# Optimization experiments

Measured on AMD Instinct MI355X. Metric: run time of the kernel, lower is better.

The kernel has to match this reference:

```python
import jax, jax.numpy as jnp
import numpy as np

N_NODES = 50000
N_EDGES = 800000
IN_DIM = 128
HIDDEN = 128
N_GRAPHS = 512


def setup_inputs() -> dict:
    key = jax.random.key(0)
    ks = jax.random.split(key, 9)
    x = jax.random.normal(ks[0], (N_NODES, IN_DIM), dtype=jnp.float32)
    edge_index = jax.random.randint(ks[1], (2, N_EDGES), 0, N_NODES, dtype=jnp.int32)
    batch = jnp.sort(jax.random.randint(ks[2], (N_NODES,), 0, N_GRAPHS, dtype=jnp.int32))
    # GCNConv params: linear (no bias) applied before propagation, bias added after.
    s1 = 1.0 / np.sqrt(IN_DIM)
    s2 = 1.0 / np.sqrt(HIDDEN)
    W1 = jax.random.uniform(ks[3], (IN_DIM, HIDDEN), jnp.float32, -s1, s1)
    b1 = jnp.zeros((HIDDEN,), jnp.float32)
    W2 = jax.random.uniform(ks[4], (HIDDEN, HIDDEN), jnp.float32, -s2, s2)
    b2 = jnp.zeros((HIDDEN,), jnp.float32)
    Wl = jax.random.uniform(ks[5], (HIDDEN, 1), jnp.float32, -s2, s2)
    bl = jax.random.uniform(ks[6], (1,), jnp.float32, -s2, s2)
    return {"x": x, "edge_index": edge_index, "batch": batch,
            "W1": W1, "b1": b1, "W2": W2, "b2": b2, "Wl": Wl, "bl": bl}


def gcn_conv(x, W, b, src, dst):
    # PyG GCNConv: h = D^{-1/2} (A + I) D^{-1/2} (x W) + b, with self-loops.
    h = x @ W                                        # [N, H]
    deg = jnp.zeros((N_NODES,), h.dtype).at[dst].add(1.0) + 1.0  # +1 for self-loop
    dinv = jax.lax.rsqrt(deg)                        # [N]
    msg = h[src] * (dinv[src] * dinv[dst])[:, None]  # [E, H] gather + normalize
    agg = jax.ops.segment_sum(msg, dst, num_segments=N_NODES)    # scatter-add
    agg = agg + h * (dinv * dinv)[:, None]           # self-loop contribution
    return agg + b


def reference(x, edge_index, batch, W1, b1, W2, b2, Wl, bl):
    src, dst = edge_index[0], edge_index[1]
    h = jax.nn.relu(gcn_conv(x, W1, b1, src, dst))
    h = jax.nn.relu(gcn_conv(h, W2, b2, src, dst))
    # global mean pool over graphs
    sums = jax.ops.segment_sum(h, batch, num_segments=N_GRAPHS)  # [G, H]
    cnt = jax.ops.segment_sum(jnp.ones((N_NODES,), h.dtype), batch, num_segments=N_GRAPHS)
    pooled = sums / jnp.maximum(cnt, 1.0)[:, None]
    return pooled @ Wl + bl
```

## Files before the change

kernel.cpp:

```cpp
#include <hip/hip_runtime.h>
#include <hip/hip_bf16.h>

#define N_NODES 50000
#define N_EDGES 800000
#define DIM 128
#define N_GRAPHS 512
#define NBUCK ((N_NODES + 63) / 64)
#define SC_CH 16384

typedef unsigned int uint;
typedef unsigned short ushort;
typedef __attribute__((ext_vector_type(8))) short short8;
typedef __attribute__((ext_vector_type(4))) float f32x4;

__device__ __forceinline__ ushort f2bf(float f) {
    uint u = __float_as_uint(f);
    uint r = (u + 0x7FFF + ((u >> 16) & 1)) >> 16;
    return (ushort)r;
}
__device__ __forceinline__ uint pack2(float a, float b) {
    return (uint)f2bf(a) | ((uint)f2bf(b) << 16);
}
__device__ __forceinline__ float2 unpack2(uint v) {
    return make_float2(__uint_as_float(v << 16), __uint_as_float(v & 0xFFFF0000u));
}


__global__ __launch_bounds__(256) void k_init(const float* __restrict__ W1,
                                              const float* __restrict__ W2,
                                              uint* __restrict__ wf1,
                                              uint* __restrict__ wf2,
                                              int* __restrict__ bucketCnt) {
    int t = blockIdx.x * 256 + threadIdx.x;
    if (t < NBUCK) bucketCnt[t] = 0;
    const float* W = (t < 8192) ? W1 : W2;
    uint* dst = (t < 8192) ? wf1 : wf2;
    int r = t & 8191;
    int j2 = r & 3;
    int lane = (r >> 2) & 63;
    int tk = r >> 8;
    int kc = tk & 3, ct = tk >> 2;
    int j = j2 * 2;
    int k = kc * 32 + (lane >> 4) * 8 + j;
    int n = ct * 16 + (lane & 15);
    dst[r] = pack2(W[k * 128 + n], W[(k + 1) * 128 + n]);
}


__global__ __launch_bounds__(1024) void k_bcount(const int* __restrict__ ei,
                                                 int* __restrict__ bucketCnt, int E) {
    __shared__ int h[NBUCK];
    int tid = threadIdx.x;
    for (int t = tid; t < NBUCK; t += 1024) h[t] = 0;
    __syncthreads();
    for (int e = blockIdx.x * 1024 + tid; e < E; e += gridDim.x * 1024)
        atomicAdd(&h[ei[E + e] >> 6], 1);
    __syncthreads();
    for (int t = tid; t < NBUCK; t += 1024) {
        int c = h[t];
        if (c) atomicAdd(&bucketCnt[t], c);
    }
}

__global__ __launch_bounds__(1024) void k_bscan(const int* __restrict__ bucketCnt,
                                                int* __restrict__ bucketStart,
                                                int* __restrict__ bucketCursor) {
    __shared__ int wsum[16];
    int tid = threadIdx.x;
    int lane = tid & 63, wv = tid >> 6;
    int v = (tid < NBUCK) ? bucketCnt[tid] : 0;
    int s = v;
    #pragma unroll
    for (int off = 1; off < 64; off <<= 1) {
        int u = __shfl_up(s, off, 64);
        if (lane >= off) s += u;
    }
    if (lane == 63) wsum[wv] = s;
    __syncthreads();
    int woff = 0;
    #pragma unroll
    for (int w = 0; w < 16; ++w) woff += (w < wv) ? wsum[w] : 0;
    int excl = woff + s - v;
    if (tid < NBUCK) {
        bucketStart[tid] = excl;
        bucketCursor[tid] = excl;
    }
    if (tid == 1023) {
        int tot = 0;
        #pragma unroll
        for (int w = 0; w < 16; ++w) tot += wsum[w];
        bucketStart[NBUCK] = tot;
    }
}

__global__ __launch_bounds__(1024) void k_bscatter(const int* __restrict__ ei,
                                                   int* __restrict__ bucketCursor,
                                                   uint* __restrict__ epk, int E) {
    __shared__ int hc[NBUCK];
    __shared__ int hbase[NBUCK];
    int tid = threadIdx.x;
    int e0 = blockIdx.x * SC_CH;
    int e1 = min(e0 + SC_CH, E);
    for (int t = tid; t < NBUCK; t += 1024) hc[t] = 0;
    __syncthreads();
    for (int e = e0 + tid; e < e1; e += 1024)
        atomicAdd(&hc[ei[E + e] >> 6], 1);
    __syncthreads();
    for (int t = tid; t < NBUCK; t += 1024) {
        int c = hc[t];
        hbase[t] = c ? atomicAdd(&bucketCursor[t], c) : 0;
        hc[t] = 0;
    }
    __syncthreads();
    for (int e = e0 + tid; e < e1; e += 1024) {
        int s = ei[e], d = ei[E + e];
        int b = d >> 6;
        int off = atomicAdd(&hc[b], 1);
        epk[hbase[b] + off] = (uint)s | ((uint)(d & 63) << 16);
    }
}

__global__ __launch_bounds__(256) void k_localcsr(const uint* __restrict__ epk,
                                                  const int* __restrict__ bucketStart,
                                                  int* __restrict__ rowStart,
                                                  float* __restrict__ dinv,
                                                  int* __restrict__ csr) {
    __shared__ int cnt[64];
    __shared__ int cur[64];
    int tid = threadIdx.x;
    int b = blockIdx.x;
    int b0 = b << 6;
    int s = bucketStart[b], e = bucketStart[b + 1];
    if (tid < 64) cnt[tid] = 0;
    __syncthreads();
    for (int i = s + tid; i < e; i += 256)
        atomicAdd(&cnt[epk[i] >> 16], 1);
    __syncthreads();
    if (tid < 64) {
        int c = cnt[tid];
        int sc = c;
        #pragma unroll
        for (int off = 1; off < 64; off <<= 1) {
            int u = __shfl_up(sc, off, 64);
            if (tid >= off) sc += u;
        }
        int excl = sc - c;
        int node = b0 + tid;
        if (node < N_NODES) {
            rowStart[node] = s + excl;
            dinv[node] = rsqrtf((float)c + 1.0f);
        }
        cur[tid] = s + excl;
    }
    if (tid == 0 && b == NBUCK - 1) rowStart[N_NODES] = e;
    __syncthreads();
    for (int i = s + tid; i < e; i += 256) {
        uint p = epk[i];
        int pos = atomicAdd(&cur[p >> 16], 1);
        csr[pos] = (int)(p & 0xFFFFu);
    }
}


template<bool BF16IN>
__global__ __launch_bounds__(256) void k_lin_mfma(const void* __restrict__ Xv,
                                                  const uint* __restrict__ Wfrag,
                                                  const float* __restrict__ dinv,
                                                  uint* __restrict__ out, int N) {
    int wv = threadIdx.x >> 6, lane = threadIdx.x & 63;
    int strip = blockIdx.x * 4 + wv;
    int row0 = strip * 16;
    if (row0 >= N) return;
    int m = lane & 15;
    int kg = lane >> 4;
    int arow = row0 + m;
    bool valid = arow < N;

    short8 af[4];
    if constexpr (!BF16IN) {
        const float* X = (const float*)Xv;
        const float* base = X + (size_t)arow * DIM + kg * 8;
        #pragma unroll
        for (int kc = 0; kc < 4; ++kc) {
            float4 a0 = make_float4(0.f, 0.f, 0.f, 0.f), a1 = a0;
            if (valid) {
                a0 = *(const float4*)(base + kc * 32);
                a1 = *(const float4*)(base + kc * 32 + 4);
            }
            short8 f;
            f[0] = (short)f2bf(a0.x); f[1] = (short)f2bf(a0.y);
            f[2] = (short)f2bf(a0.z); f[3] = (short)f2bf(a0.w);
            f[4] = (short)f2bf(a1.x); f[5] = (short)f2bf(a1.y);
            f[6] = (short)f2bf(a1.z); f[7] = (short)f2bf(a1.w);
            af[kc] = f;
        }
    } else {
        const uint* X = (const uint*)Xv;
        const uint* base = X + (size_t)arow * 64 + kg * 4;
        #pragma unroll
        for (int kc = 0; kc < 4; ++kc) {
            union { uint4 u; short8 s; } cv;
            cv.u = valid ? *(const uint4*)(base + kc * 16) : make_uint4(0, 0, 0, 0);
            af[kc] = cv.s;
        }
    }

    f32x4 acc[8];
    #pragma unroll
    for (int ct = 0; ct < 8; ++ct) acc[ct] = (f32x4){0.f, 0.f, 0.f, 0.f};

    #pragma unroll
    for (int ct = 0; ct < 8; ++ct) {
        #pragma unroll
        for (int kc = 0; kc < 4; ++kc) {
            union { uint4 u; short8 s; } bv;
            bv.u = *(const uint4*)(Wfrag + ((size_t)(ct * 4 + kc) * 64 + lane) * 4);
            acc[ct] = __builtin_amdgcn_mfma_f32_16x16x32_bf16(af[kc], bv.s, acc[ct], 0, 0, 0);
        }
    }

    ushort* ob = (ushort*)out;
    #pragma unroll
    for (int reg = 0; reg < 4; ++reg) {
        int orow = row0 + kg * 4 + reg;
        if (orow < N) {
            float di = dinv[orow];
            size_t rb = (size_t)orow * DIM + m;
            #pragma unroll
            for (int ct = 0; ct < 8; ++ct)
                ob[rb + ct * 16] = f2bf(acc[ct][reg] * di);
        }
    }
}


template<bool FUSE_HEAD>
__global__ __launch_bounds__(256) void k_aggregate(const uint* __restrict__ HS,
                                                   const int* __restrict__ rowStart,
                                                   const int* __restrict__ csr,
                                                   const float* __restrict__ dinv,
                                                   const float* __restrict__ bias,
                                                   const float* __restrict__ Wl,
                                                   uint* __restrict__ outRow,
                                                   float* __restrict__ outY, int n) {
    int wv = threadIdx.x >> 6, lane = threadIdx.x & 63;
    int nid = blockIdx.x * 4 + wv;
    if (nid >= n) return;
    float2 acc = unpack2(HS[(size_t)nid * 64 + lane]);
    int beg = rowStart[nid], end = rowStart[nid + 1];
    int e = beg;
    for (; e + 7 < end; e += 8) {
        int s0 = csr[e],     s1 = csr[e + 1], s2 = csr[e + 2], s3 = csr[e + 3];
        int s4 = csr[e + 4], s5 = csr[e + 5], s6 = csr[e + 6], s7 = csr[e + 7];
        float2 f0 = unpack2(HS[(size_t)s0 * 64 + lane]);
        float2 f1 = unpack2(HS[(size_t)s1 * 64 + lane]);
        float2 f2 = unpack2(HS[(size_t)s2 * 64 + lane]);
        float2 f3 = unpack2(HS[(size_t)s3 * 64 + lane]);
        float2 f4 = unpack2(HS[(size_t)s4 * 64 + lane]);
        float2 f5 = unpack2(HS[(size_t)s5 * 64 + lane]);
        float2 f6 = unpack2(HS[(size_t)s6 * 64 + lane]);
        float2 f7 = unpack2(HS[(size_t)s7 * 64 + lane]);
        acc.x += ((f0.x + f1.x) + (f2.x + f3.x)) + ((f4.x + f5.x) + (f6.x + f7.x));
        acc.y += ((f0.y + f1.y) + (f2.y + f3.y)) + ((f4.y + f5.y) + (f6.y + f7.y));
    }
    for (; e + 1 < end; e += 2) {
        int s0 = csr[e], s1 = csr[e + 1];
        float2 f0 = unpack2(HS[(size_t)s0 * 64 + lane]);
        float2 f1 = unpack2(HS[(size_t)s1 * 64 + lane]);
        acc.x += f0.x + f1.x;
        acc.y += f0.y + f1.y;
    }
    if (e < end) {
        float2 f0 = unpack2(HS[(size_t)csr[e] * 64 + lane]);
        acc.x += f0.x;
        acc.y += f0.y;
    }
    float di = dinv[nid];
    int c = lane * 2;
    float ox = fmaxf(acc.x * di + bias[c], 0.f);
    float oy = fmaxf(acc.y * di + bias[c + 1], 0.f);
    if constexpr (!FUSE_HEAD) {
        outRow[(size_t)nid * 64 + lane] = pack2(ox, oy);
    } else {
        float part = ox * Wl[c] + oy * Wl[c + 1];
        #pragma unroll
        for (int off = 32; off > 0; off >>= 1) part += __shfl_down(part, off, 64);
        if (lane == 0) outY[nid] = part;
    }
}


__global__ __launch_bounds__(64) void k_pool_y(const float* __restrict__ y,
                                               const int* __restrict__ batch,
                                               const float* __restrict__ bl,
                                               float* __restrict__ out, int n) {
    int g = blockIdx.x;
    int lane = threadIdx.x;
    int lo = 0, hi = n;
    while (lo < hi) { int mid = (lo + hi) >> 1; if (batch[mid] < g) lo = mid + 1; else hi = mid; }
    int s = lo;
    hi = n;
    while (lo < hi) { int mid = (lo + hi) >> 1; if (batch[mid] < g + 1) lo = mid + 1; else hi = mid; }
    int e = lo;

    float sum = 0.f;
    for (int i = s + lane; i < e; i += 64) sum += y[i];
    #pragma unroll
    for (int off = 32; off > 0; off >>= 1) sum += __shfl_down(sum, off, 64);
    if (lane == 0) out[g] = sum / fmaxf((float)(e - s), 1.0f) + bl[0];
}


extern "C" void kernel_launch(void* const* d_in, const int* in_sizes, int n_in,
                              void* d_out, int out_size, void* d_ws, size_t ws_size,
                              hipStream_t stream) {
    const float* x  = (const float*)d_in[0];
    const int*   ei = (const int*)d_in[1];
    const int*   batch = (const int*)d_in[2];
    const float* W1 = (const float*)d_in[3];
    const float* b1 = (const float*)d_in[4];
    const float* W2 = (const float*)d_in[5];
    const float* b2 = (const float*)d_in[6];
    const float* Wl = (const float*)d_in[7];
    const float* bl = (const float*)d_in[8];
    float* out = (float*)d_out;

    uint* hs  = (uint*)d_ws;
    uint* h2b = hs + (size_t)N_NODES * 64;
    float* dinv = (float*)(h2b + (size_t)N_NODES * 64);
    float* ynode = dinv + N_NODES;
    int* rowStart = (int*)(ynode + N_NODES);
    int* bucketCnt = rowStart + N_NODES + 4;
    int* bucketStart = bucketCnt + 784;
    int* bucketCursor = bucketStart + 784;
    int* csr = bucketCursor + 784;
    uint* epk = (uint*)(csr + N_EDGES);
    uint* wf1 = epk + N_EDGES;
    uint* wf2 = wf1 + 8192;

    k_init<<<64, 256, 0, stream>>>(W1, W2, wf1, wf2, bucketCnt);

    k_bcount<<<64, 1024, 0, stream>>>(ei, bucketCnt, N_EDGES);
    k_bscan<<<1, 1024, 0, stream>>>(bucketCnt, bucketStart, bucketCursor);
    k_bscatter<<<(N_EDGES + SC_CH - 1) / SC_CH, 1024, 0, stream>>>(ei, bucketCursor, epk, N_EDGES);
    k_localcsr<<<NBUCK, 256, 0, stream>>>(epk, bucketStart, rowStart, dinv, csr);

    int strips = (N_NODES + 15) / 16;
    int gemmGrid = (strips + 3) / 4;
    int aggGrid  = (N_NODES + 3) / 4;

    k_lin_mfma<false><<<gemmGrid, 256, 0, stream>>>(x, wf1, dinv, hs, N_NODES);
    k_aggregate<false><<<aggGrid, 256, 0, stream>>>(hs, rowStart, csr, dinv, b1, Wl, h2b, ynode, N_NODES);

    k_lin_mfma<true><<<gemmGrid, 256, 0, stream>>>(h2b, wf2, dinv, hs, N_NODES);
    k_aggregate<true><<<aggGrid, 256, 0, stream>>>(hs, rowStart, csr, dinv, b2, Wl, h2b, ynode, N_NODES);

    k_pool_y<<<N_GRAPHS, 64, 0, stream>>>(ynode, batch, bl, out, N_NODES);
}
```

Baseline: 151.8 us.

## Fuse CSR build with first GEMM in one kernel using grid barriers

The four CSR-construction kernels are merged into 64 blocks of a single persistent kernel that use a software global barrier between phases. The same launch runs the first-layer GEMM on 782 more blocks, so the GEMM overlaps with the CSR build. Because that GEMM can no longer depend on dinv, the source-side normalization moves into the first aggregation, which multiplies each neighbour's features by a gathered dinv. This removes several launches and serialization points, at the cost of extra dinv gathers and a spin barrier that can deadlock if the 64 CSR blocks are not all resident at once.

```diff
diff --git a/kernel.cpp b/kernel.cpp
--- a/kernel.cpp
+++ b/kernel.cpp
@@ -6,7 +6,9 @@
 #define DIM 128
 #define N_GRAPHS 512
 #define NBUCK ((N_NODES + 63) / 64)
-#define SC_CH 16384
+#define CSR_BLOCKS 64
+#define EPB (N_EDGES / CSR_BLOCKS)
+#define GEMM_BLOCKS 782
 
 typedef unsigned int uint;
 typedef unsigned short ushort;
@@ -30,9 +32,11 @@
                                               const float* __restrict__ W2,
                                               uint* __restrict__ wf1,
                                               uint* __restrict__ wf2,
-                                              int* __restrict__ bucketCnt) {
+                                              int* __restrict__ bucketCnt,
+                                              int* __restrict__ bar) {
     int t = blockIdx.x * 256 + threadIdx.x;
     if (t < NBUCK) bucketCnt[t] = 0;
+    if (t >= NBUCK && t < NBUCK + 2) bar[t - NBUCK] = 0;
     const float* W = (t < 8192) ? W1 : W2;
     uint* dst = (t < 8192) ? wf1 : wf2;
     int r = t & 8191;
@@ -47,128 +51,32 @@
 }
 
 
-__global__ __launch_bounds__(1024) void k_bcount(const int* __restrict__ ei,
-                                                 int* __restrict__ bucketCnt, int E) {
-    __shared__ int h[NBUCK];
-    int tid = threadIdx.x;
-    for (int t = tid; t < NBUCK; t += 1024) h[t] = 0;
-    __syncthreads();
-    for (int e = blockIdx.x * 1024 + tid; e < E; e += gridDim.x * 1024)
-        atomicAdd(&h[ei[E + e] >> 6], 1);
-    __syncthreads();
-    for (int t = tid; t < NBUCK; t += 1024) {
-        int c = h[t];
-        if (c) atomicAdd(&bucketCnt[t], c);
-    }
-}
-
-__global__ __launch_bounds__(1024) void k_bscan(const int* __restrict__ bucketCnt,
-                                                int* __restrict__ bucketStart,
-                                                int* __restrict__ bucketCursor) {
-    __shared__ int wsum[16];
-    int tid = threadIdx.x;
-    int lane = tid & 63, wv = tid >> 6;
-    int v = (tid < NBUCK) ? bucketCnt[tid] : 0;
-    int s = v;
-    #pragma unroll
-    for (int off = 1; off < 64; off <<= 1) {
-        int u = __shfl_up(s, off, 64);
-        if (lane >= off) s += u;
-    }
-    if (lane == 63) wsum[wv] = s;
-    __syncthreads();
-    int woff = 0;
-    #pragma unroll
-    for (int w = 0; w < 16; ++w) woff += (w < wv) ? wsum[w] : 0;
-    int excl = woff + s - v;
-    if (tid < NBUCK) {
-        bucketStart[tid] = excl;
-        bucketCursor[tid] = excl;
-    }
-    if (tid == 1023) {
-        int tot = 0;
-        #pragma unroll
-        for (int w = 0; w < 16; ++w) tot += wsum[w];
-        bucketStart[NBUCK] = tot;
-    }
-}
-
-__global__ __launch_bounds__(1024) void k_bscatter(const int* __restrict__ ei,
-                                                   int* __restrict__ bucketCursor,
-                                                   uint* __restrict__ epk, int E) {
-    __shared__ int hc[NBUCK];
-    __shared__ int hbase[NBUCK];
-    int tid = threadIdx.x;
-    int e0 = blockIdx.x * SC_CH;
-    int e1 = min(e0 + SC_CH, E);
-    for (int t = tid; t < NBUCK; t += 1024) hc[t] = 0;
-    __syncthreads();
-    for (int e = e0 + tid; e < e1; e += 1024)
-        atomicAdd(&hc[ei[E + e] >> 6], 1);
-    __syncthreads();
-    for (int t = tid; t < NBUCK; t += 1024) {
-        int c = hc[t];
-        hbase[t] = c ? atomicAdd(&bucketCursor[t], c) : 0;
-        hc[t] = 0;
-    }
-    __syncthreads();
-    for (int e = e0 + tid; e < e1; e += 1024) {
-        int s = ei[e], d = ei[E + e];
-        int b = d >> 6;
-        int off = atomicAdd(&hc[b], 1);
-        epk[hbase[b] + off] = (uint)s | ((uint)(d & 63) << 16);
-    }
-}
-
-__global__ __launch_bounds__(256) void k_localcsr(const uint* __restrict__ epk,
-                                                  const int* __restrict__ bucketStart,
-                                                  int* __restrict__ rowStart,
-                                                  float* __restrict__ dinv,
-                                                  int* __restrict__ csr) {
-    __shared__ int cnt[64];
-    __shared__ int cur[64];
-    int tid = threadIdx.x;
-    int b = blockIdx.x;
-    int b0 = b << 6;
-    int s = bucketStart[b], e = bucketStart[b + 1];
-    if (tid < 64) cnt[tid] = 0;
-    __syncthreads();
-    for (int i = s + tid; i < e; i += 256)
-        atomicAdd(&cnt[epk[i] >> 16], 1);
-    __syncthreads();
-    if (tid < 64) {
-        int c = cnt[tid];
-        int sc = c;
-        #pragma unroll
-        for (int off = 1; off < 64; off <<= 1) {
-            int u = __shfl_up(sc, off, 64);
-            if (tid >= off) sc += u;
-        }
-        int excl = sc - c;
-        int node = b0 + tid;
-        if (node < N_NODES) {
-            rowStart[node] = s + excl;
-            dinv[node] = rsqrtf((float)c + 1.0f);
-        }
-        cur[tid] = s + excl;
-    }
-    if (tid == 0 && b == NBUCK - 1) rowStart[N_NODES] = e;
-    __syncthreads();
-    for (int i = s + tid; i < e; i += 256) {
-        uint p = epk[i];
-        int pos = atomicAdd(&cur[p >> 16], 1);
-        csr[pos] = (int)(p & 0xFFFFu);
-    }
-}
-
-
-template<bool BF16IN>
-__global__ __launch_bounds__(256) void k_lin_mfma(const void* __restrict__ Xv,
-                                                  const uint* __restrict__ Wfrag,
-                                                  const float* __restrict__ dinv,
-                                                  uint* __restrict__ out, int N) {
+__device__ __forceinline__ void gbar64(int* barCnt, int* barGen, int phase) {
+    __syncthreads();
+    if (threadIdx.x == 0) {
+        __threadfence();
+        if (atomicAdd(barCnt, 1) == CSR_BLOCKS - 1) {
+            atomicExch(barCnt, 0);
+            __threadfence();
+            atomicAdd(barGen, 1);
+        } else {
+            while (atomicAdd(barGen, 0) <= phase) {
+                __builtin_amdgcn_s_sleep(2);
+            }
+        }
+        __threadfence();
+    }
+    __syncthreads();
+}
+
+
+template<bool BF16IN, bool SCALE>
+__device__ __forceinline__ void gemm_body(int blk, const void* __restrict__ Xv,
+                                          const uint* __restrict__ Wfrag,
+                                          const float* __restrict__ dinv,
+                                          uint* __restrict__ out, int N) {
     int wv = threadIdx.x >> 6, lane = threadIdx.x & 63;
-    int strip = blockIdx.x * 4 + wv;
+    int strip = blk * 4 + wv;
     int row0 = strip * 16;
     if (row0 >= N) return;
     int m = lane & 15;
@@ -224,17 +132,153 @@
     for (int reg = 0; reg < 4; ++reg) {
         int orow = row0 + kg * 4 + reg;
         if (orow < N) {
-            float di = dinv[orow];
+            float di = SCALE ? dinv[orow] : 1.0f;
             size_t rb = (size_t)orow * DIM + m;
             #pragma unroll
             for (int ct = 0; ct < 8; ++ct)
-                ob[rb + ct * 16] = f2bf(acc[ct][reg] * di);
-        }
-    }
-}
-
-
-template<bool FUSE_HEAD>
+                ob[rb + ct * 16] = f2bf(SCALE ? acc[ct][reg] * di : acc[ct][reg]);
+        }
+    }
+}
+
+
+__global__ __launch_bounds__(256) void k_mega(const float* __restrict__ x,
+                                              const uint* __restrict__ wf1,
+                                              uint* __restrict__ hs,
+                                              const int* __restrict__ ei,
+                                              int* __restrict__ bucketCnt,
+                                              int* __restrict__ bucketStart,
+                                              int* __restrict__ bucketCursor,
+                                              uint* __restrict__ epk,
+                                              int* __restrict__ rowStart,
+                                              float* __restrict__ dinv_w,
+                                              int* __restrict__ csr,
+                                              int* __restrict__ bar) {
+    if (blockIdx.x >= CSR_BLOCKS) {
+        gemm_body<false, false>(blockIdx.x - CSR_BLOCKS, x, wf1, nullptr, hs, N_NODES);
+        return;
+    }
+    int cb = blockIdx.x;
+    int tid = threadIdx.x;
+    int* barCnt = bar;
+    int* barGen = bar + 1;
+    __shared__ int sh[2 * NBUCK];
+    __shared__ int wsum4[4];
+    __shared__ int cnt[64];
+    __shared__ int cur[64];
+    int e0 = cb * EPB, e1 = e0 + EPB;
+
+    int* h = sh;
+    for (int t = tid; t < NBUCK; t += 256) h[t] = 0;
+    __syncthreads();
+    for (int e = e0 + tid; e < e1; e += 256)
+        atomicAdd(&h[ei[N_EDGES + e] >> 6], 1);
+    __syncthreads();
+    for (int t = tid; t < NBUCK; t += 256) {
+        int c = h[t];
+        if (c) atomicAdd(&bucketCnt[t], c);
+    }
+    gbar64(barCnt, barGen, 0);
+
+    if (cb == 0) {
+        int base = tid * 4;
+        int v[4]; int tot = 0;
+        #pragma unroll
+        for (int i = 0; i < 4; ++i) {
+            v[i] = (base + i < NBUCK) ? bucketCnt[base + i] : 0;
+            tot += v[i];
+        }
+        int lane = tid & 63, w = tid >> 6;
+        int sc = tot;
+        #pragma unroll
+        for (int off = 1; off < 64; off <<= 1) {
+            int u = __shfl_up(sc, off, 64);
+            if (lane >= off) sc += u;
+        }
+        if (lane == 63) wsum4[w] = sc;
+        __syncthreads();
+        int woff = 0;
+        #pragma unroll
+        for (int ww = 0; ww < 4; ++ww) woff += (ww < w) ? wsum4[ww] : 0;
+        int run = woff + sc - tot;
+        #pragma unroll
+        for (int i = 0; i < 4; ++i) {
+            if (base + i < NBUCK) {
+                bucketStart[base + i] = run;
+                bucketCursor[base + i] = run;
+            }
+            run += v[i];
+        }
+        if (tid == 255) bucketStart[NBUCK] = run;
+    }
+    gbar64(barCnt, barGen, 1);
+
+    int* hc = sh;
+    int* hbase = sh + NBUCK;
+    for (int t = tid; t < NBUCK; t += 256) hc[t] = 0;
+    __syncthreads();
+    for (int e = e0 + tid; e < e1; e += 256)
+        atomicAdd(&hc[ei[N_EDGES + e] >> 6], 1);
+    __syncthreads();
+    for (int t = tid; t < NBUCK; t += 256) {
+        int c = hc[t];
+        hbase[t] = c ? atomicAdd(&bucketCursor[t], c) : 0;
+        hc[t] = 0;
+    }
+    __syncthreads();
+    for (int e = e0 + tid; e < e1; e += 256) {
+        int s = ei[e], d = ei[N_EDGES + e];
+        int b = d >> 6;
+        int off = atomicAdd(&hc[b], 1);
+        epk[hbase[b] + off] = (uint)s | ((uint)(d & 63) << 16);
+    }
+    gbar64(barCnt, barGen, 2);
+
+    for (int b = cb; b < NBUCK; b += CSR_BLOCKS) {
+        int b0 = b << 6;
+        int s = bucketStart[b], e = bucketStart[b + 1];
+        if (tid < 64) cnt[tid] = 0;
+        __syncthreads();
+        for (int i = s + tid; i < e; i += 256)
+            atomicAdd(&cnt[epk[i] >> 16], 1);
+        __syncthreads();
+        if (tid < 64) {
+            int c = cnt[tid];
+            int sc = c;
+            #pragma unroll
+            for (int off = 1; off < 64; off <<= 1) {
+                int u = __shfl_up(sc, off, 64);
+                if (tid >= off) sc += u;
+            }
+            int excl = sc - c;
+            int node = b0 + tid;
+            if (node < N_NODES) {
+                rowStart[node] = s + excl;
+                dinv_w[node] = rsqrtf((float)c + 1.0f);
+            }
+            cur[tid] = s + excl;
+        }
+        if (tid == 0 && b == NBUCK - 1) rowStart[N_NODES] = e;
+        __syncthreads();
+        for (int i = s + tid; i < e; i += 256) {
+            uint p = epk[i];
+            int pos = atomicAdd(&cur[p >> 16], 1);
+            csr[pos] = (int)(p & 0xFFFFu);
+        }
+        __syncthreads();
+    }
+}
+
+
+__global__ __launch_bounds__(256) void k_lin2(const uint* __restrict__ Xb,
+                                              const uint* __restrict__ Wfrag,
+                                              const float* __restrict__ dinv,
+                                              uint* __restrict__ out, int N) {
+    gemm_body<true, true>(blockIdx.x, Xb, Wfrag, dinv, out, N);
+}
+
+
+template<bool FUSE_HEAD, bool SCALE_SRC>
 __global__ __launch_bounds__(256) void k_aggregate(const uint* __restrict__ HS,
                                                    const int* __restrict__ rowStart,
                                                    const int* __restrict__ csr,
@@ -246,7 +290,11 @@
     int wv = threadIdx.x >> 6, lane = threadIdx.x & 63;
     int nid = blockIdx.x * 4 + wv;
     if (nid >= n) return;
-    float2 acc = unpack2(HS[(size_t)nid * 64 + lane]);
+    float di = dinv[nid];
+    float2 self = unpack2(HS[(size_t)nid * 64 + lane]);
+    float2 acc;
+    if constexpr (SCALE_SRC) { acc.x = self.x * di; acc.y = self.y * di; }
+    else                     { acc = self; }
     int beg = rowStart[nid], end = rowStart[nid + 1];
     int e = beg;
     for (; e + 7 < end; e += 8) {
@@ -260,22 +308,30 @@
         float2 f5 = unpack2(HS[(size_t)s5 * 64 + lane]);
         float2 f6 = unpack2(HS[(size_t)s6 * 64 + lane]);
         float2 f7 = unpack2(HS[(size_t)s7 * 64 + lane]);
-        acc.x += ((f0.x + f1.x) + (f2.x + f3.x)) + ((f4.x + f5.x) + (f6.x + f7.x));
-        acc.y += ((f0.y + f1.y) + (f2.y + f3.y)) + ((f4.y + f5.y) + (f6.y + f7.y));
-    }
-    for (; e + 1 < end; e += 2) {
-        int s0 = csr[e], s1 = csr[e + 1];
+        if constexpr (SCALE_SRC) {
+            float d0 = dinv[s0], d1 = dinv[s1], d2 = dinv[s2], d3 = dinv[s3];
+            float d4 = dinv[s4], d5 = dinv[s5], d6 = dinv[s6], d7 = dinv[s7];
+            acc.x += ((f0.x * d0 + f1.x * d1) + (f2.x * d2 + f3.x * d3))
+                   + ((f4.x * d4 + f5.x * d5) + (f6.x * d6 + f7.x * d7));
+            acc.y += ((f0.y * d0 + f1.y * d1) + (f2.y * d2 + f3.y * d3))
+                   + ((f4.y * d4 + f5.y * d5) + (f6.y * d6 + f7.y * d7));
+        } else {
+            acc.x += ((f0.x + f1.x) + (f2.x + f3.x)) + ((f4.x + f5.x) + (f6.x + f7.x));
+            acc.y += ((f0.y + f1.y) + (f2.y + f3.y)) + ((f4.y + f5.y) + (f6.y + f7.y));
+        }
+    }
+    for (; e < end; ++e) {
+        int s0 = csr[e];
         float2 f0 = unpack2(HS[(size_t)s0 * 64 + lane]);
-        float2 f1 = unpack2(HS[(size_t)s1 * 64 + lane]);
-        acc.x += f0.x + f1.x;
-        acc.y += f0.y + f1.y;
-    }
-    if (e < end) {
-        float2 f0 = unpack2(HS[(size_t)csr[e] * 64 + lane]);
-        acc.x += f0.x;
-        acc.y += f0.y;
-    }
-    float di = dinv[nid];
+        if constexpr (SCALE_SRC) {
+            float d0 = dinv[s0];
+            acc.x += f0.x * d0;
+            acc.y += f0.y * d0;
+        } else {
+            acc.x += f0.x;
+            acc.y += f0.y;
+        }
+    }
     int c = lane * 2;
     float ox = fmaxf(acc.x * di + bias[c], 0.f);
     float oy = fmaxf(acc.y * di + bias[c + 1], 0.f);
@@ -333,27 +389,26 @@
     int* bucketCnt = rowStart + N_NODES + 4;
     int* bucketStart = bucketCnt + 784;
     int* bucketCursor = bucketStart + 784;
-    int* csr = bucketCursor + 784;
+    int* bar = bucketCursor + 784;
+    int* csr = bar + 4;
     uint* epk = (uint*)(csr + N_EDGES);
     uint* wf1 = epk + N_EDGES;
     uint* wf2 = wf1 + 8192;
 
-    k_init<<<64, 256, 0, stream>>>(W1, W2, wf1, wf2, bucketCnt);
-
-    k_bcount<<<64, 1024, 0, stream>>>(ei, bucketCnt, N_EDGES);
-    k_bscan<<<1, 1024, 0, stream>>>(bucketCnt, bucketStart, bucketCursor);
-    k_bscatter<<<(N_EDGES + SC_CH - 1) / SC_CH, 1024, 0, stream>>>(ei, bucketCursor, epk, N_EDGES);
-    k_localcsr<<<NBUCK, 256, 0, stream>>>(epk, bucketStart, rowStart, dinv, csr);
-
-    int strips = (N_NODES + 15) / 16;
-    int gemmGrid = (strips + 3) / 4;
-    int aggGrid  = (N_NODES + 3) / 4;
-
-    k_lin_mfma<false><<<gemmGrid, 256, 0, stream>>>(x, wf1, dinv, hs, N_NODES);
-    k_aggregate<false><<<aggGrid, 256, 0, stream>>>(hs, rowStart, csr, dinv, b1, Wl, h2b, ynode, N_NODES);
-
-    k_lin_mfma<true><<<gemmGrid, 256, 0, stream>>>(h2b, wf2, dinv, hs, N_NODES);
-    k_aggregate<true><<<aggGrid, 256, 0, stream>>>(hs, rowStart, csr, dinv, b2, Wl, h2b, ynode, N_NODES);
+    k_init<<<64, 256, 0, stream>>>(W1, W2, wf1, wf2, bucketCnt, bar);
+
+    k_mega<<<CSR_BLOCKS + GEMM_BLOCKS, 256, 0, stream>>>(
+        x, wf1, hs, ei, bucketCnt, bucketStart, bucketCursor,
+        epk, rowStart, dinv, csr, bar);
+
+    int aggGrid = (N_NODES + 3) / 4;
+
+    k_aggregate<false, true><<<aggGrid, 256, 0, stream>>>(
+        hs, rowStart, csr, dinv, b1, Wl, h2b, ynode, N_NODES);
+
+    k_lin2<<<GEMM_BLOCKS, 256, 0, stream>>>(h2b, wf2, dinv, hs, N_NODES);
+    k_aggregate<true, false><<<aggGrid, 256, 0, stream>>>(
+        hs, rowStart, csr, dinv, b2, Wl, h2b, ynode, N_NODES);
 
     k_pool_y<<<N_GRAPHS, 64, 0, stream>>>(ynode, batch, bl, out, N_NODES);
 }
```

After: 211.0 us. 39.0% more time.
